# Performance work log

Hardware: AMD Instinct MI355X
Metric: run time of the kernel (lower is better)

The kernel has to match this reference:

```python
import jax, jax.numpy as jnp
import numpy as np

N0, N1, N2 = 100000, 25000, 6250
E0, E1, E2 = 600000, 150000, 40000
K = 6
NUM_CLASSES = 10


def setup_inputs() -> dict:
    key = jax.random.key(0)
    ks = jax.random.split(key, 20)
    inp = {
        "pos": jax.random.normal(ks[0], (N0, 3), dtype=jnp.float32),
        "edge_index0": jax.random.randint(ks[1], (2, E0), 0, N0, dtype=jnp.int32),
        "edge_index1": jax.random.randint(ks[2], (2, E1), 0, N1, dtype=jnp.int32),
        "edge_index2": jax.random.randint(ks[3], (2, E2), 0, N2, dtype=jnp.int32),
        "d0_rows": jax.random.randint(ks[4], (N0,), 0, N1, dtype=jnp.int32),
        "d0_cols": jax.random.randint(ks[5], (N0,), 0, N0, dtype=jnp.int32),
        "d0_vals": jax.random.uniform(ks[6], (N0,), dtype=jnp.float32),
        "d1_rows": jax.random.randint(ks[7], (N1,), 0, N2, dtype=jnp.int32),
        "d1_cols": jax.random.randint(ks[8], (N1,), 0, N1, dtype=jnp.int32),
        "d1_vals": jax.random.uniform(ks[9], (N1,), dtype=jnp.float32),
        "W0": jax.random.normal(ks[10], (K, 3, 32), dtype=jnp.float32) * 0.1,
        "b0": jax.random.normal(ks[11], (32,), dtype=jnp.float32) * 0.1,
        "W1": jax.random.normal(ks[12], (K, 32, 64), dtype=jnp.float32) * 0.1,
        "b1": jax.random.normal(ks[13], (64,), dtype=jnp.float32) * 0.1,
        "W2": jax.random.normal(ks[14], (K, 64, 128), dtype=jnp.float32) * 0.1,
        "b2": jax.random.normal(ks[15], (128,), dtype=jnp.float32) * 0.1,
        "lin_w": jax.random.normal(ks[16], (NUM_CLASSES, N2 * 128), dtype=jnp.float32) * 0.01,
        "lin_b": jax.random.normal(ks[17], (NUM_CLASSES,), dtype=jnp.float32) * 0.1,
    }
    return inp


def _cheb_edge_weights(row, col, n):
    # PyG get_laplacian(sym) followed by 2L/lambda_max - I with lambda_max=2:
    # diagonal becomes 0, off-diagonal weight = -deg^{-1/2}[row] * deg^{-1/2}[col]
    deg = jax.ops.segment_sum(jnp.ones(row.shape[0], jnp.float32), row, num_segments=n)
    dinv = jnp.where(deg > 0, 1.0 / jnp.sqrt(deg), 0.0)
    return -dinv[row] * dinv[col]


def _cheb_conv(x, edge_index, W, b, n):
    # Chebyshev recurrence: Tx0 = x, Tx1 = L_hat x, Tx_k = 2 L_hat Tx_{k-1} - Tx_{k-2}
    row, col = edge_index[0], edge_index[1]
    w = _cheb_edge_weights(row, col, n)

    def prop(z):  # [n, C] -> [n, C] scatter-gather over edges
        return jax.ops.segment_sum(w[:, None] * z[col], row, num_segments=n)

    Tx0 = x
    out = Tx0 @ W[0]
    Tx1 = prop(x)
    out = out + Tx1 @ W[1]
    for k in range(2, W.shape[0]):
        Tx2 = 2.0 * prop(Tx1) - Tx0
        out = out + Tx2 @ W[k]
        Tx0, Tx1 = Tx1, Tx2
    return out + b


def _pool(x, rows, cols, vals, n_out):
    # torch.sparse.mm(D, x) with D given in COO form
    return jax.ops.segment_sum(vals[:, None] * x[cols], rows, num_segments=n_out)


def reference(pos, edge_index0, edge_index1, edge_index2,
              d0_rows, d0_cols, d0_vals, d1_rows, d1_cols, d1_vals,
              W0, b0, W1, b1, W2, b2, lin_w, lin_b):
    x = jax.nn.relu(_cheb_conv(pos, edge_index0, W0, b0, N0))
    x = _pool(x, d0_rows, d0_cols, d0_vals, N1)
    x = jax.nn.relu(_cheb_conv(x, edge_index1, W1, b1, N1))
    x = _pool(x, d1_rows, d1_cols, d1_vals, N2)
    x = _cheb_conv(x, edge_index2, W2, b2, N2)  # no ReLU on last conv
    Z = lin_w @ x.reshape(-1) + lin_b
    return Z
```

## Files before the change

kernel.cpp:

```cpp
#include <hip/hip_runtime.h>


#define TPB 256
#define NB   318
#define BCAP 8192
#define EPB  4096
#define TXS  800000LL

static inline int gs(long long n) { return (int)((n + TPB - 1) / TPB); }

struct Desc5 {
    const int* rows[5];
    const int* cols[5];
    const float* vals[5];
    int eoff[6];
    int doff[5];
};


__global__ void k_binA_pad(Desc5 d, int* __restrict__ gbcnt, int2* __restrict__ binrec,
                           int Etot, int binBlocks,
                           const float* __restrict__ pos, float4* __restrict__ pdst,
                           int npos) {
    __shared__ int2 srec[EPB];
    __shared__ unsigned short sbuck[EPB];
    __shared__ int scnt[NB], sbase[NB], slcur[NB];
    int tid = threadIdx.x;
    if ((int)blockIdx.x >= binBlocks) {
        int i = (blockIdx.x - binBlocks) * 256 + tid;
        if (i < npos)
            pdst[i] = make_float4(pos[3 * i], pos[3 * i + 1], pos[3 * i + 2], 0.f);
        return;
    }
    int e0 = blockIdx.x * EPB;
    int ne = min(EPB, Etot - e0);
    for (int b = tid; b < NB; b += 256) scnt[b] = 0;
    __syncthreads();
    for (int i = tid; i < ne; i += 256) {
        int e = e0 + i;
        int s = 0;
        while (e >= d.eoff[s + 1]) ++s;
        int le = e - d.eoff[s];
        int grow = d.doff[s] + d.rows[s][le];
        int col = d.cols[s][le];
        int vb = (s >= 3) ? __float_as_int(d.vals[s][le]) : 0;
        int b = grow >> 9;
        srec[i] = make_int2(((grow & 511) << 17) | col, vb);
        sbuck[i] = (unsigned short)b;
        atomicAdd(&scnt[b], 1);
    }
    __syncthreads();
    for (int b = tid; b < NB; b += 256) {
        sbase[b] = scnt[b] > 0 ? atomicAdd(&gbcnt[b], scnt[b]) : 0;
        slcur[b] = 0;
    }
    __syncthreads();
    for (int i = tid; i < ne; i += 256) {
        int b = sbuck[i];
        int off = atomicAdd(&slcur[b], 1);
        binrec[(long long)b * BCAP + sbase[b] + off] = srec[i];
    }
}

__global__ void k_B1(const int* __restrict__ gbcnt, const int2* __restrict__ binrec,
                     int* __restrict__ rowptr, float* __restrict__ dinv,
                     int ntot, int ndinv, int Etot) {
    __shared__ int cnt[512], lexcl[512], wsum[4];
    int bucket = blockIdx.x, tid = threadIdx.x;
    int lane = tid & 63, wid = tid >> 6;
    {
        int v0 = (2 * tid < NB) ? gbcnt[2 * tid] : 0;
        int v1 = (2 * tid + 1 < NB) ? gbcnt[2 * tid + 1] : 0;
        int p = v0 + v1;
        int s = p;
#pragma unroll
        for (int off = 1; off < 64; off <<= 1) {
            int t = __shfl_up(s, off, 64);
            if (lane >= off) s += t;
        }
        if (lane == 63) wsum[wid] = s;
        __syncthreads();
        int add = 0;
        for (int w = 0; w < wid; ++w) add += wsum[w];
        int ep = add + s - p;
        lexcl[2 * tid] = ep; lexcl[2 * tid + 1] = ep + v0;
        __syncthreads();
    }
    int base = lexcl[bucket];
    __syncthreads();
    int ne = gbcnt[bucket];
    const int2* br = binrec + (long long)bucket * BCAP;
    cnt[2 * tid] = 0; cnt[2 * tid + 1] = 0;
    __syncthreads();
    for (int i = tid; i < ne; i += 256)
        atomicAdd(&cnt[br[i].x >> 17], 1);
    __syncthreads();
    int c0 = cnt[2 * tid], c1 = cnt[2 * tid + 1], p = c0 + c1;
    int s = p;
#pragma unroll
    for (int off = 1; off < 64; off <<= 1) {
        int t = __shfl_up(s, off, 64);
        if (lane >= off) s += t;
    }
    if (lane == 63) wsum[wid] = s;
    __syncthreads();
    int add = 0;
    for (int w = 0; w < wid; ++w) add += wsum[w];
    int ep = add + s - p;
    lexcl[2 * tid] = ep; lexcl[2 * tid + 1] = ep + c0;
    __syncthreads();
    int row0 = bucket << 9;
    int nrows = min(512, ntot - row0);
    for (int lr = tid; lr < nrows; lr += 256) {
        int grow = row0 + lr;
        rowptr[grow] = base + lexcl[lr];
        if (grow < ndinv) {
            int c = cnt[lr];
            dinv[grow] = c > 0 ? 1.0f / sqrtf((float)c) : 0.f;
        }
    }
    if (bucket == 0 && tid == 0) rowptr[ntot] = Etot;
}

__global__ void k_B2(const int* __restrict__ gbcnt, const int2* __restrict__ binrec,
                     const int* __restrict__ rowptr, const float* __restrict__ dinv,
                     int2* __restrict__ rec, int ntot) {
    __shared__ int lbase[512], lcur[512];
    int bucket = blockIdx.x, tid = threadIdx.x;
    int row0 = bucket << 9;
    for (int i = tid; i < 512; i += 256) {
        int grow = row0 + i;
        lbase[i] = (grow < ntot) ? rowptr[grow] : 0;
        lcur[i] = 0;
    }
    __syncthreads();
    int ne = gbcnt[bucket];
    const int2* br = binrec + (long long)bucket * BCAP;
    for (int i = tid; i < ne; i += 256) {
        int2 r = br[i];
        int lr = r.x >> 17, col = r.x & 0x1FFFF;
        int grow = row0 + lr;
        int pos = lbase[lr] + atomicAdd(&lcur[lr], 1);
        float wv;
        if (grow < 100000)      wv = dinv[col];
        else if (grow < 125000) wv = dinv[100000 + col];
        else if (grow < 131250) wv = dinv[125000 + col];
        else                    wv = __int_as_float(r.y);
        rec[pos] = make_int2(col, __float_as_int(wv));
    }
}


__global__ void k_sprop_c4p(const int* __restrict__ rowptr, const int2* __restrict__ rec,
                            const float* __restrict__ dinv, const float* __restrict__ src,
                            const float* __restrict__ prev, float* __restrict__ dst,
                            int n, int mode) {
    int idx = blockIdx.x * blockDim.x + threadIdx.x;
    if (idx >= 2 * n) return;
    int r = idx >> 1, half = idx & 1;
    int s0 = rowptr[r], s1 = rowptr[r + 1];
    float4 a0 = make_float4(0.f, 0.f, 0.f, 0.f), a1 = a0;
    int j = s0 + half;
    for (; j + 2 < s1; j += 4) {
        int2 r0 = rec[j], r1 = rec[j + 2];
        float w0 = __int_as_float(r0.y), w1 = __int_as_float(r1.y);
        float4 s0v = *(const float4*)(src + (long long)r0.x * 4);
        float4 s1v = *(const float4*)(src + (long long)r1.x * 4);
        a0.x += w0 * s0v.x; a0.y += w0 * s0v.y; a0.z += w0 * s0v.z; a0.w += w0 * s0v.w;
        a1.x += w1 * s1v.x; a1.y += w1 * s1v.y; a1.z += w1 * s1v.z; a1.w += w1 * s1v.w;
    }
    if (j < s1) {
        int2 rr = rec[j];
        float w = __int_as_float(rr.y);
        float4 s = *(const float4*)(src + (long long)rr.x * 4);
        a0.x += w * s.x; a0.y += w * s.y; a0.z += w * s.z; a0.w += w * s.w;
    }
    a0.x += a1.x; a0.y += a1.y; a0.z += a1.z; a0.w += a1.w;
    a0.x += __shfl_xor(a0.x, 1, 64);
    a0.y += __shfl_xor(a0.y, 1, 64);
    a0.z += __shfl_xor(a0.z, 1, 64);
    a0.w += __shfl_xor(a0.w, 1, 64);
    if (half == 0) {
        float m = -dinv[r];
        long long o = (long long)r * 4;
        float4 out;
        if (mode) {
            float4 p = *(const float4*)(prev + o);
            out.x = 2.f * m * a0.x - p.x; out.y = 2.f * m * a0.y - p.y;
            out.z = 2.f * m * a0.z - p.z; out.w = 2.f * m * a0.w - p.w;
        } else {
            out.x = m * a0.x; out.y = m * a0.y; out.z = m * a0.z; out.w = m * a0.w;
        }
        *(float4*)(dst + o) = out;
    }
}

__device__ __forceinline__
void sprop32p_body(const int* __restrict__ rowptr, const int2* __restrict__ rec,
                   const float* __restrict__ dinv, const float* __restrict__ src,
                   const float* __restrict__ prev, float* __restrict__ dst,
                   int n, int mode, int idx) {
    constexpr int C = 32;
    if (idx >= n * 8) return;
    int cid = idx >> 1, half = idx & 1;
    int r = cid >> 2, c4 = (cid & 3) * 8;
    int s0 = rowptr[r], s1 = rowptr[r + 1];
    float4 a0 = make_float4(0.f, 0.f, 0.f, 0.f), a1 = a0;
    for (int j = s0 + half; j < s1; j += 2) {
        int2 rr = rec[j];
        float w = __int_as_float(rr.y);
        const float* sp = src + (long long)rr.x * C + c4;
        float4 s0v = *(const float4*)(sp);
        float4 s1v = *(const float4*)(sp + 4);
        a0.x += w * s0v.x; a0.y += w * s0v.y; a0.z += w * s0v.z; a0.w += w * s0v.w;
        a1.x += w * s1v.x; a1.y += w * s1v.y; a1.z += w * s1v.z; a1.w += w * s1v.w;
    }
    a0.x += __shfl_xor(a0.x, 1, 64); a0.y += __shfl_xor(a0.y, 1, 64);
    a0.z += __shfl_xor(a0.z, 1, 64); a0.w += __shfl_xor(a0.w, 1, 64);
    a1.x += __shfl_xor(a1.x, 1, 64); a1.y += __shfl_xor(a1.y, 1, 64);
    a1.z += __shfl_xor(a1.z, 1, 64); a1.w += __shfl_xor(a1.w, 1, 64);
    if (half == 0) {
        float m = -dinv[r];
        long long o = (long long)r * C + c4;
        float4 o0, o1;
        if (mode) {
            float4 p0 = *(const float4*)(prev + o);
            float4 p1 = *(const float4*)(prev + o + 4);
            o0.x = 2.f * m * a0.x - p0.x; o0.y = 2.f * m * a0.y - p0.y;
            o0.z = 2.f * m * a0.z - p0.z; o0.w = 2.f * m * a0.w - p0.w;
            o1.x = 2.f * m * a1.x - p1.x; o1.y = 2.f * m * a1.y - p1.y;
            o1.z = 2.f * m * a1.z - p1.z; o1.w = 2.f * m * a1.w - p1.w;
        } else {
            o0.x = m * a0.x; o0.y = m * a0.y; o0.z = m * a0.z; o0.w = m * a0.w;
            o1.x = m * a1.x; o1.y = m * a1.y; o1.z = m * a1.z; o1.w = m * a1.w;
        }
        *(float4*)(dst + o) = o0;
        *(float4*)(dst + o + 4) = o1;
    }
}

__device__ __forceinline__
void sprop64p_body(const int* __restrict__ rowptr, const int2* __restrict__ rec,
                   const float* __restrict__ dinv, const float* __restrict__ src,
                   const float* __restrict__ prev, float* __restrict__ dst,
                   int n, int mode, int idx) {
    constexpr int C = 64, C4 = 16;
    if (idx >= n * C4 * 2) return;
    int cid = idx >> 1, half = idx & 1;
    int r = cid / C4, c4 = (cid - r * C4) * 4;
    int s0 = rowptr[r], s1 = rowptr[r + 1];
    float4 a0 = make_float4(0.f, 0.f, 0.f, 0.f), a1 = a0;
    int j = s0 + half;
    for (; j + 2 < s1; j += 4) {
        int2 r0 = rec[j], r1 = rec[j + 2];
        float w0 = __int_as_float(r0.y), w1 = __int_as_float(r1.y);
        float4 s0v = *(const float4*)(src + (long long)r0.x * C + c4);
        float4 s1v = *(const float4*)(src + (long long)r1.x * C + c4);
        a0.x += w0 * s0v.x; a0.y += w0 * s0v.y; a0.z += w0 * s0v.z; a0.w += w0 * s0v.w;
        a1.x += w1 * s1v.x; a1.y += w1 * s1v.y; a1.z += w1 * s1v.z; a1.w += w1 * s1v.w;
    }
    if (j < s1) {
        int2 rr = rec[j];
        float w = __int_as_float(rr.y);
        float4 s = *(const float4*)(src + (long long)rr.x * C + c4);
        a0.x += w * s.x; a0.y += w * s.y; a0.z += w * s.z; a0.w += w * s.w;
    }
    a0.x += a1.x; a0.y += a1.y; a0.z += a1.z; a0.w += a1.w;
    a0.x += __shfl_xor(a0.x, 1, 64); a0.y += __shfl_xor(a0.y, 1, 64);
    a0.z += __shfl_xor(a0.z, 1, 64); a0.w += __shfl_xor(a0.w, 1, 64);
    if (half == 0) {
        float m = -dinv[r];
        long long o = (long long)r * C + c4;
        float4 out;
        if (mode) {
            float4 p = *(const float4*)(prev + o);
            out.x = 2.f * m * a0.x - p.x; out.y = 2.f * m * a0.y - p.y;
            out.z = 2.f * m * a0.z - p.z; out.w = 2.f * m * a0.w - p.w;
        } else {
            out.x = m * a0.x; out.y = m * a0.y; out.z = m * a0.z; out.w = m * a0.w;
        }
        *(float4*)(dst + o) = out;
    }
}


template <int CIN, int COUT, int NT>
__device__ __forceinline__
void gemm1k_body(float* __restrict__ part, const float* __restrict__ txbase,
                 const float* __restrict__ W, int n, int pstride, int kg, int idx) {
    constexpr int CO4 = COUT / 4;
    int per = (n / NT) * CO4;
    if (idx >= per) return;
    int tile = idx / CO4, co = (idx - tile * CO4) * 4;
    int node0 = tile * NT;
    float4 acc[NT];
#pragma unroll
    for (int i = 0; i < NT; ++i) acc[i] = make_float4(0.f, 0.f, 0.f, 0.f);
    const float* xb = txbase + (long long)kg * TXS + (long long)node0 * CIN;
    const float* Wk = W + (long long)kg * CIN * COUT + co;
#pragma unroll 1
    for (int c4 = 0; c4 < CIN / 4; ++c4) {
        const float* Wr = Wk + c4 * 4 * COUT;
        float4 w0 = *(const float4*)(Wr);
        float4 w1 = *(const float4*)(Wr + COUT);
        float4 w2 = *(const float4*)(Wr + 2 * COUT);
        float4 w3 = *(const float4*)(Wr + 3 * COUT);
#pragma unroll
        for (int i = 0; i < NT; ++i) {
            float4 xv = *(const float4*)(xb + i * CIN + c4 * 4);
            acc[i].x += xv.x * w0.x + xv.y * w1.x + xv.z * w2.x + xv.w * w3.x;
            acc[i].y += xv.x * w0.y + xv.y * w1.y + xv.z * w2.y + xv.w * w3.y;
            acc[i].z += xv.x * w0.z + xv.y * w1.z + xv.z * w2.z + xv.w * w3.z;
            acc[i].w += xv.x * w0.w + xv.y * w1.w + xv.z * w2.w + xv.w * w3.w;
        }
    }
    float* op = part + (long long)kg * pstride + (long long)node0 * COUT + co;
#pragma unroll
    for (int i = 0; i < NT; ++i)
        *(float4*)(op + (long long)i * COUT) = acc[i];
}


__global__ __launch_bounds__(256, 4)
void k_pack1(const int* __restrict__ rowptr, const int2* __restrict__ rec,
             const float* __restrict__ dinv, const float* __restrict__ src,
             const float* __restrict__ prev, float* __restrict__ dst,
             int n, int mode, float* __restrict__ part,
             const float* __restrict__ txbase, const float* __restrict__ W,
             int pstride, int kg, int spropBlocks) {
    int bid = blockIdx.x;
    if (bid < spropBlocks)
        sprop32p_body(rowptr, rec, dinv, src, prev, dst, n, mode,
                      bid * 256 + threadIdx.x);
    else
        gemm1k_body<32, 64, 4>(part, txbase, W, n, pstride, kg,
                               (bid - spropBlocks) * 256 + threadIdx.x);
}

__global__ __launch_bounds__(256, 4)
void k_pack2(const int* __restrict__ rowptr, const int2* __restrict__ rec,
             const float* __restrict__ dinv, const float* __restrict__ src,
             const float* __restrict__ prev, float* __restrict__ dst,
             int n, int mode, float* __restrict__ part,
             const float* __restrict__ txbase, const float* __restrict__ W,
             int pstride, int kg, int spropBlocks) {
    int bid = blockIdx.x;
    if (bid < spropBlocks)
        sprop64p_body(rowptr, rec, dinv, src, prev, dst, n, mode,
                      bid * 256 + threadIdx.x);
    else
        gemm1k_body<64, 128, 2>(part, txbase, W, n, pstride, kg,
                                (bid - spropBlocks) * 256 + threadIdx.x);
}


__device__ __forceinline__
void convf1_body(const int* __restrict__ rowptr, const int2* __restrict__ rec,
                 const float* __restrict__ dinv, const float* __restrict__ txbase,
                 const float* __restrict__ W, float* __restrict__ part,
                 int n, int pstride, int bid, float (*ltx)[36]) {
    constexpr int C = 32;
    int tid = threadIdx.x;
    int row0 = bid * 32;
    const float* src = txbase + 4 * TXS;
    const float* prv = txbase + 3 * TXS;
    {
        int rl = tid >> 3, c4 = (tid & 7) * 4;
        int r = row0 + rl;
        if (r < n) {
            int s0 = rowptr[r], s1 = rowptr[r + 1];
            float4 a0 = make_float4(0.f, 0.f, 0.f, 0.f), a1 = a0;
            int j = s0;
            for (; j + 2 <= s1; j += 2) {
                int2 q0 = rec[j], q1 = rec[j + 1];
                float w0 = __int_as_float(q0.y), w1 = __int_as_float(q1.y);
                float4 s0v = *(const float4*)(src + (long long)q0.x * C + c4);
                float4 s1v = *(const float4*)(src + (long long)q1.x * C + c4);
                a0.x += w0 * s0v.x; a0.y += w0 * s0v.y; a0.z += w0 * s0v.z; a0.w += w0 * s0v.w;
                a1.x += w1 * s1v.x; a1.y += w1 * s1v.y; a1.z += w1 * s1v.z; a1.w += w1 * s1v.w;
            }
            if (j < s1) {
                int2 q = rec[j];
                float w = __int_as_float(q.y);
                float4 s = *(const float4*)(src + (long long)q.x * C + c4);
                a0.x += w * s.x; a0.y += w * s.y; a0.z += w * s.z; a0.w += w * s.w;
            }
            a0.x += a1.x; a0.y += a1.y; a0.z += a1.z; a0.w += a1.w;
            float m = -dinv[r];
            float4 p = *(const float4*)(prv + (long long)r * C + c4);
            ltx[rl][c4]     = 2.f * m * a0.x - p.x;
            ltx[rl][c4 + 1] = 2.f * m * a0.y - p.y;
            ltx[rl][c4 + 2] = 2.f * m * a0.z - p.z;
            ltx[rl][c4 + 3] = 2.f * m * a0.w - p.w;
        }
    }
    __syncthreads();
    const float* Wk = W + 5 * 32 * 64;
#pragma unroll
    for (int half = 0; half < 2; ++half) {
        int out_id = half * 256 + tid;
        int rl = out_id >> 4, co = (out_id & 15) * 4;
        int r = row0 + rl;
        if (r >= n) continue;
        float4 acc = make_float4(0.f, 0.f, 0.f, 0.f);
#pragma unroll 1
        for (int c4 = 0; c4 < 8; ++c4) {
            const float* Wr = Wk + c4 * 4 * 64 + co;
            float4 w0 = *(const float4*)(Wr);
            float4 w1 = *(const float4*)(Wr + 64);
            float4 w2 = *(const float4*)(Wr + 128);
            float4 w3 = *(const float4*)(Wr + 192);
            float4 xv = *(const float4*)(&ltx[rl][c4 * 4]);
            acc.x += xv.x * w0.x + xv.y * w1.x + xv.z * w2.x + xv.w * w3.x;
            acc.y += xv.x * w0.y + xv.y * w1.y + xv.z * w2.y + xv.w * w3.y;
            acc.z += xv.x * w0.z + xv.y * w1.z + xv.z * w2.z + xv.w * w3.z;
            acc.w += xv.x * w0.w + xv.y * w1.w + xv.z * w2.w + xv.w * w3.w;
        }
        *(float4*)(part + 5LL * pstride + (long long)r * 64 + co) = acc;
    }
}

__device__ __forceinline__
void convf2_body(const int* __restrict__ rowptr, const int2* __restrict__ rec,
                 const float* __restrict__ dinv, const float* __restrict__ txbase,
                 const float* __restrict__ W, float* __restrict__ part,
                 int n, int pstride, int bid, float (*ltx)[68]) {
    constexpr int C = 64;
    int tid = threadIdx.x;
    int row0 = bid * 16;
    const float* src = txbase + 4 * TXS;
    const float* prv = txbase + 3 * TXS;
    {
        int rl = tid >> 4, c4 = (tid & 15) * 4;
        int r = row0 + rl;
        if (r < n) {
            int s0 = rowptr[r], s1 = rowptr[r + 1];
            float4 a0 = make_float4(0.f, 0.f, 0.f, 0.f), a1 = a0;
            int j = s0;
            for (; j + 2 <= s1; j += 2) {
                int2 q0 = rec[j], q1 = rec[j + 1];
                float w0 = __int_as_float(q0.y), w1 = __int_as_float(q1.y);
                float4 s0v = *(const float4*)(src + (long long)q0.x * C + c4);
                float4 s1v = *(const float4*)(src + (long long)q1.x * C + c4);
                a0.x += w0 * s0v.x; a0.y += w0 * s0v.y; a0.z += w0 * s0v.z; a0.w += w0 * s0v.w;
                a1.x += w1 * s1v.x; a1.y += w1 * s1v.y; a1.z += w1 * s1v.z; a1.w += w1 * s1v.w;
            }
            if (j < s1) {
                int2 q = rec[j];
                float w = __int_as_float(q.y);
                float4 s = *(const float4*)(src + (long long)q.x * C + c4);
                a0.x += w * s.x; a0.y += w * s.y; a0.z += w * s.z; a0.w += w * s.w;
            }
            a0.x += a1.x; a0.y += a1.y; a0.z += a1.z; a0.w += a1.w;
            float m = -dinv[r];
            float4 p = *(const float4*)(prv + (long long)r * C + c4);
            ltx[rl][c4]     = 2.f * m * a0.x - p.x;
            ltx[rl][c4 + 1] = 2.f * m * a0.y - p.y;
            ltx[rl][c4 + 2] = 2.f * m * a0.z - p.z;
            ltx[rl][c4 + 3] = 2.f * m * a0.w - p.w;
        }
    }
    __syncthreads();
    const float* Wk = W + 5 * 64 * 128;
#pragma unroll
    for (int half = 0; half < 2; ++half) {
        int out_id = half * 256 + tid;
        int rl = out_id >> 5, co = (out_id & 31) * 4;
        int r = row0 + rl;
        if (r >= n) continue;
        float4 acc = make_float4(0.f, 0.f, 0.f, 0.f);
#pragma unroll 1
        for (int c4 = 0; c4 < 16; ++c4) {
            const float* Wr = Wk + c4 * 4 * 128 + co;
            float4 w0 = *(const float4*)(Wr);
            float4 w1 = *(const float4*)(Wr + 128);
            float4 w2 = *(const float4*)(Wr + 256);
            float4 w3 = *(const float4*)(Wr + 384);
            float4 xv = *(const float4*)(&ltx[rl][c4 * 4]);
            acc.x += xv.x * w0.x + xv.y * w1.x + xv.z * w2.x + xv.w * w3.x;
            acc.y += xv.x * w0.y + xv.y * w1.y + xv.z * w2.y + xv.w * w3.y;
            acc.z += xv.x * w0.z + xv.y * w1.z + xv.z * w2.z + xv.w * w3.z;
            acc.w += xv.x * w0.w + xv.y * w1.w + xv.z * w2.w + xv.w * w3.w;
        }
        *(float4*)(part + 5LL * pstride + (long long)r * 128 + co) = acc;
    }
}

__global__ __launch_bounds__(256, 4)
void k_packf1(const int* __restrict__ rowptr, const int2* __restrict__ rec,
              const float* __restrict__ dinv, const float* __restrict__ txbase,
              const float* __restrict__ W, float* __restrict__ part,
              int n, int pstride, int fB) {
    __shared__ float ltx[32][36];
    int bid = blockIdx.x;
    if (bid < fB)
        convf1_body(rowptr, rec, dinv, txbase, W, part, n, pstride, bid, ltx);
    else
        gemm1k_body<32, 64, 4>(part, txbase, W, n, pstride, 4,
                               (bid - fB) * 256 + threadIdx.x);
}

__global__ __launch_bounds__(256, 4)
void k_packf2(const int* __restrict__ rowptr, const int2* __restrict__ rec,
              const float* __restrict__ dinv, const float* __restrict__ txbase,
              const float* __restrict__ W, float* __restrict__ part,
              int n, int pstride, int fB) {
    __shared__ float ltx[16][68];
    int bid = blockIdx.x;
    if (bid < fB)
        convf2_body(rowptr, rec, dinv, txbase, W, part, n, pstride, bid, ltx);
    else
        gemm1k_body<64, 128, 2>(part, txbase, W, n, pstride, 4,
                                (bid - fB) * 256 + threadIdx.x);
}

__global__ __launch_bounds__(256, 4)
void k_conv0_final(const int* __restrict__ rowptr, const int2* __restrict__ rec,
                   const float* __restrict__ dinv, const float* __restrict__ txbase,
                   const float* __restrict__ W, const float* __restrict__ b,
                   float* __restrict__ out, int n) {
    int r = blockIdx.x * blockDim.x + threadIdx.x;
    if (r >= n) return;
    const float* src = txbase + 4 * TXS;
    int s0 = rowptr[r], s1 = rowptr[r + 1];
    float4 a0 = make_float4(0.f, 0.f, 0.f, 0.f);
    float4 a1 = a0;
    int j = s0;
    if ((j & 1) && j < s1) {
        int2 rr = rec[j];
        float w = __int_as_float(rr.y);
        float4 s = *(const float4*)(src + (long long)rr.x * 4);
        a0.x += w * s.x; a0.y += w * s.y; a0.z += w * s.z;
        ++j;
    }
    for (; j + 2 <= s1; j += 2) {
        int4 q = *(const int4*)(rec + j);
        float wa = __int_as_float(q.y), wb = __int_as_float(q.w);
        float4 sa = *(const float4*)(src + (long long)q.x * 4);
        float4 sb = *(const float4*)(src + (long long)q.z * 4);
        a0.x += wa * sa.x; a0.y += wa * sa.y; a0.z += wa * sa.z;
        a1.x += wb * sb.x; a1.y += wb * sb.y; a1.z += wb * sb.z;
    }
    if (j < s1) {
        int2 rr = rec[j];
        float w = __int_as_float(rr.y);
        float4 s = *(const float4*)(src + (long long)rr.x * 4);
        a0.x += w * s.x; a0.y += w * s.y; a0.z += w * s.z;
    }
    a0.x += a1.x; a0.y += a1.y; a0.z += a1.z;
    float m = -dinv[r];
    float4 xv[6];
#pragma unroll
    for (int k = 0; k < 5; ++k)
        xv[k] = *(const float4*)(txbase + (long long)k * TXS + (long long)r * 4);
    xv[5].x = 2.f * m * a0.x - xv[3].x;
    xv[5].y = 2.f * m * a0.y - xv[3].y;
    xv[5].z = 2.f * m * a0.z - xv[3].z;
    float* op = out + (long long)r * 32;
#pragma unroll 1
    for (int co4 = 0; co4 < 8; ++co4) {
        float4 acc = *(const float4*)(b + co4 * 4);
#pragma unroll
        for (int k = 0; k < 6; ++k) {
            const float* Wk = W + k * 96 + co4 * 4;
            float4 w0 = *(const float4*)(Wk);
            float4 w1 = *(const float4*)(Wk + 32);
            float4 w2 = *(const float4*)(Wk + 64);
            acc.x += xv[k].x * w0.x + xv[k].y * w1.x + xv[k].z * w2.x;
            acc.y += xv[k].x * w0.y + xv[k].y * w1.y + xv[k].z * w2.y;
            acc.z += xv[k].x * w0.z + xv[k].y * w1.z + xv[k].z * w2.z;
            acc.w += xv[k].x * w0.w + xv[k].y * w1.w + xv[k].z * w2.w;
        }
        *(float4*)(op + co4 * 4) = acc;
    }
}


template <int C>
__global__ void k_spool4_t(const int* __restrict__ rowptr, const int2* __restrict__ rec,
                           const float* __restrict__ x, float* __restrict__ out, int n) {
    constexpr int C4 = C / 4;
    int idx = blockIdx.x * blockDim.x + threadIdx.x;
    if (idx >= n * C4) return;
    int r = idx / C4, c4 = (idx - r * C4) * 4;
    int s0 = rowptr[r], s1 = rowptr[r + 1];
    float4 acca = make_float4(0.f, 0.f, 0.f, 0.f);
    float4 accb = make_float4(0.f, 0.f, 0.f, 0.f);
    int j = s0;
    if ((j & 1) && j < s1) {
        int2 rr = rec[j];
        float v = __int_as_float(rr.y);
        float4 s = *(const float4*)(x + (long long)rr.x * C + c4);
        acca.x += v * fmaxf(s.x, 0.f); acca.y += v * fmaxf(s.y, 0.f);
        acca.z += v * fmaxf(s.z, 0.f); acca.w += v * fmaxf(s.w, 0.f);
        ++j;
    }
    for (; j + 2 <= s1; j += 2) {
        int4 q = *(const int4*)(rec + j);
        float va = __int_as_float(q.y), vb = __int_as_float(q.w);
        float4 sa = *(const float4*)(x + (long long)q.x * C + c4);
        float4 sb = *(const float4*)(x + (long long)q.z * C + c4);
        acca.x += va * fmaxf(sa.x, 0.f); acca.y += va * fmaxf(sa.y, 0.f);
        acca.z += va * fmaxf(sa.z, 0.f); acca.w += va * fmaxf(sa.w, 0.f);
        accb.x += vb * fmaxf(sb.x, 0.f); accb.y += vb * fmaxf(sb.y, 0.f);
        accb.z += vb * fmaxf(sb.z, 0.f); accb.w += vb * fmaxf(sb.w, 0.f);
    }
    if (j < s1) {
        int2 rr = rec[j];
        float v = __int_as_float(rr.y);
        float4 s = *(const float4*)(x + (long long)rr.x * C + c4);
        acca.x += v * fmaxf(s.x, 0.f); acca.y += v * fmaxf(s.y, 0.f);
        acca.z += v * fmaxf(s.z, 0.f); acca.w += v * fmaxf(s.w, 0.f);
    }
    acca.x += accb.x; acca.y += accb.y; acca.z += accb.z; acca.w += accb.w;
    *(float4*)(out + (long long)r * C + c4) = acca;
}


template <int C, int KSPLIT>
__global__ void k_pool_f(const int* __restrict__ rowptr, const int2* __restrict__ rec,
                         const float* __restrict__ part, const float* __restrict__ bias,
                         float* __restrict__ out, int n, int partStride) {
    constexpr int C4 = C / 4;
    int idx = blockIdx.x * blockDim.x + threadIdx.x;
    if (idx >= n * C4) return;
    int r = idx / C4, c4 = (idx - r * C4) * 4;
    int s0 = rowptr[r], s1 = rowptr[r + 1];
    float4 bb = *(const float4*)(bias + c4);
    float4 acc = make_float4(0.f, 0.f, 0.f, 0.f);
    for (int j = s0; j < s1; ++j) {
        int2 rr = rec[j];
        float v = __int_as_float(rr.y);
        float4 x = bb;
#pragma unroll
        for (int s = 0; s < KSPLIT; ++s) {
            float4 p = *(const float4*)(part + (long long)s * partStride + (long long)rr.x * C + c4);
            x.x += p.x; x.y += p.y; x.z += p.z; x.w += p.w;
        }
        acc.x += v * fmaxf(x.x, 0.f); acc.y += v * fmaxf(x.y, 0.f);
        acc.z += v * fmaxf(x.z, 0.f); acc.w += v * fmaxf(x.w, 0.f);
    }
    *(float4*)(out + (long long)r * C + c4) = acc;
}


__global__ void k_linear_partial_f(const float* __restrict__ lw,
                                   const float4* __restrict__ part,
                                   const float* __restrict__ b2,
                                   float* __restrict__ partials,
                                   int len4, int len, int nblk) {
    float acc[10];
#pragma unroll
    for (int j = 0; j < 10; ++j) acc[j] = 0.f;
    const float4* b2v = (const float4*)b2;
    for (int i = blockIdx.x * blockDim.x + threadIdx.x; i < len4;
         i += gridDim.x * blockDim.x) {
        float4 xv = b2v[i & 31];
#pragma unroll
        for (int s = 0; s < 6; ++s) {
            float4 p = part[s * 200000 + i];
            xv.x += p.x; xv.y += p.y; xv.z += p.z; xv.w += p.w;
        }
#pragma unroll
        for (int j = 0; j < 10; ++j) {
            float4 wv = *(const float4*)(lw + (long long)j * len + i * 4);
            acc[j] += xv.x * wv.x + xv.y * wv.y + xv.z * wv.z + xv.w * wv.w;
        }
    }
    __shared__ float lds[4][10];
    int wid = threadIdx.x >> 6, lane = threadIdx.x & 63;
#pragma unroll
    for (int j = 0; j < 10; ++j) {
        float v = acc[j];
        for (int off = 32; off > 0; off >>= 1) v += __shfl_down(v, off, 64);
        if (lane == 0) lds[wid][j] = v;
    }
    __syncthreads();
    if (threadIdx.x < 10) {
        float s = lds[0][threadIdx.x] + lds[1][threadIdx.x] +
                  lds[2][threadIdx.x] + lds[3][threadIdx.x];
        partials[threadIdx.x * nblk + blockIdx.x] = s;
    }
}

__global__ void k_linear_final(const float* __restrict__ partials,
                               const float* __restrict__ lb,
                               float* __restrict__ out, int nblk) {
    int j = threadIdx.x >> 6, lane = threadIdx.x & 63;
    float v = 0.f;
    for (int b = lane; b < nblk; b += 64) v += partials[j * nblk + b];
    for (int off = 32; off > 0; off >>= 1) v += __shfl_down(v, off, 64);
    if (lane == 0) out[j] = lb[j] + v;
}

extern "C" void kernel_launch(void* const* d_in, const int* in_sizes, int n_in,
                              void* d_out, int out_size, void* d_ws, size_t ws_size,
                              hipStream_t stream) {
    const int cN0 = 100000, cN1 = 25000, cN2 = 6250;
    const int cE0 = 600000, cE1 = 150000, cE2 = 40000;
    const int NBLK = 512;

    const float* pos = (const float*)d_in[0];
    const int*   ei0 = (const int*)d_in[1];
    const int*   ei1 = (const int*)d_in[2];
    const int*   ei2 = (const int*)d_in[3];
    const int*   d0r = (const int*)d_in[4];
    const int*   d0c = (const int*)d_in[5];
    const float* d0v = (const float*)d_in[6];
    const int*   d1r = (const int*)d_in[7];
    const int*   d1c = (const int*)d_in[8];
    const float* d1v = (const float*)d_in[9];
    const float* W0  = (const float*)d_in[10];
    const float* b0  = (const float*)d_in[11];
    const float* W1  = (const float*)d_in[12];
    const float* b1  = (const float*)d_in[13];
    const float* W2  = (const float*)d_in[14];
    const float* b2  = (const float*)d_in[15];
    const float* lw  = (const float*)d_in[16];
    const float* lb  = (const float*)d_in[17];
    float* outZ = (float*)d_out;

    const int ntot = cN0 + cN1 + cN2 + cN1 + cN2;
    const int Etot = cE0 + cE1 + cE2 + cN0 + cN1;
    const int Eg   = cE0 + cE1 + cE2;
    const int ndinv = cN0 + cN1 + cN2;
    const int doff0 = 0, doff1 = cN0, doff2 = cN0 + cN1,
              doffp0 = doff2 + cN2, doffp1 = doffp0 + cN1;

    int*   iws    = (int*)d_ws;
    int*   gbcnt  = iws;
    int*   rowptr = gbcnt + 320;
    float* dinv   = (float*)(rowptr + 162504);
    int2*  binrec = (int2*)(dinv + 131256);
    int2*  rec    = binrec + (long long)NB * BCAP;
    float* txbuf  = (float*)(rec + 915000);
    float* part   = txbuf + 6 * TXS;
    float* bufOut = part + 9600000;
    float* lpart  = bufOut + 3200000;

    Desc5 d;
    d.rows[0] = ei0;        d.cols[0] = ei0 + cE0; d.vals[0] = nullptr;
    d.rows[1] = ei1;        d.cols[1] = ei1 + cE1; d.vals[1] = nullptr;
    d.rows[2] = ei2;        d.cols[2] = ei2 + cE2; d.vals[2] = nullptr;
    d.rows[3] = d0r;        d.cols[3] = d0c;       d.vals[3] = d0v;
    d.rows[4] = d1r;        d.cols[4] = d1c;       d.vals[4] = d1v;
    d.eoff[0] = 0;
    d.eoff[1] = cE0;
    d.eoff[2] = cE0 + cE1;
    d.eoff[3] = Eg;
    d.eoff[4] = Eg + cN0;
    d.eoff[5] = Etot;
    d.doff[0] = doff0; d.doff[1] = doff1; d.doff[2] = doff2;
    d.doff[3] = doffp0; d.doff[4] = doffp1;

    hipMemsetAsync(gbcnt, 0, (size_t)NB * 4, stream);
    int binBlocks = (Etot + EPB - 1) / EPB;
    int padBlocks = gs(cN0);
    k_binA_pad<<<binBlocks + padBlocks, TPB, 0, stream>>>(
        d, gbcnt, binrec, Etot, binBlocks, pos, (float4*)txbuf, cN0);
    k_B1<<<NB, TPB, 0, stream>>>(gbcnt, binrec, rowptr, dinv, ntot, ndinv, Etot);
    k_B2<<<NB, TPB, 0, stream>>>(gbcnt, binrec, rowptr, dinv, rec, ntot);

    for (int k = 1; k <= 4; ++k) {
        const float* src = txbuf + (long long)(k - 1) * TXS;
        const float* prev = (k >= 2) ? txbuf + (long long)(k - 2) * TXS : nullptr;
        float* dst = txbuf + (long long)k * TXS;
        k_sprop_c4p<<<gs((long long)cN0 * 2), TPB, 0, stream>>>(
            rowptr + doff0, rec, dinv + doff0, src, prev, dst, cN0, k >= 2 ? 1 : 0);
    }
    k_conv0_final<<<gs(cN0), TPB, 0, stream>>>(
        rowptr + doff0, rec, dinv + doff0, txbuf, W0, b0, bufOut, cN0);
    k_spool4_t<32><<<gs((long long)cN1 * 8), TPB, 0, stream>>>(
        rowptr + doffp0, rec, bufOut, txbuf, cN1);

    {
        const int pstride = cN1 * 64;
        int sB = gs((long long)cN1 * 8);
        int gB = gs((long long)(cN1 / 4) * 16);
        for (int k = 1; k <= 4; ++k) {
            const float* src = txbuf + (long long)(k - 1) * TXS;
            const float* prev = (k >= 2) ? txbuf + (long long)(k - 2) * TXS : nullptr;
            float* dst = txbuf + (long long)k * TXS;
            k_pack1<<<sB + gB, TPB, 0, stream>>>(
                rowptr + doff1, rec, dinv + doff1, src, prev, dst, cN1,
                k >= 2 ? 1 : 0, part, txbuf, W1, pstride, k - 1, sB);
        }
        int fB = (cN1 + 31) / 32;
        k_packf1<<<fB + gB, TPB, 0, stream>>>(
            rowptr + doff1, rec, dinv + doff1, txbuf, W1, part, cN1, pstride, fB);
        k_pool_f<64, 6><<<gs((long long)cN2 * 16), TPB, 0, stream>>>(
            rowptr + doffp1, rec, part, b1, txbuf, cN2, pstride);
    }

    {
        const int pstride = cN2 * 128;
        int sB = gs((long long)cN2 * 32);
        int gB = gs((long long)(cN2 / 2) * 32);
        for (int k = 1; k <= 4; ++k) {
            const float* src = txbuf + (long long)(k - 1) * TXS;
            const float* prev = (k >= 2) ? txbuf + (long long)(k - 2) * TXS : nullptr;
            float* dst = txbuf + (long long)k * TXS;
            k_pack2<<<sB + gB, TPB, 0, stream>>>(
                rowptr + doff2, rec, dinv + doff2, src, prev, dst, cN2,
                k >= 2 ? 1 : 0, part, txbuf, W2, pstride, k - 1, sB);
        }
        int fB = (cN2 + 15) / 16;
        k_packf2<<<fB + gB, TPB, 0, stream>>>(
            rowptr + doff2, rec, dinv + doff2, txbuf, W2, part, cN2, pstride, fB);
        k_linear_partial_f<<<NBLK, TPB, 0, stream>>>(
            lw, (const float4*)part, b2, lpart, cN2 * 128 / 4, cN2 * 128, NBLK);
        k_linear_final<<<1, 640, 0, stream>>>(lpart, lb, outZ, NBLK);
    }
}
```

Measured before the change: 253.0 us.

## Overlap tail of CSR record build with first level-0 propagation; fuse linear reduction

The record-scatter kernel is split so that the buckets past B2SPLIT (which hold later graph levels and pooling records) run in the same launch as the first Chebyshev propagation for level 0. This overlaps the two kernels' work and removes one launch. The final linear layer now does its cross-block reduction in a last-block-done pattern using an atomic counter, replacing the separate single-block final kernel. The overlap depends on level-0 rows living entirely in buckets below B2SPLIT, and the counter needs the widened memset.

```diff
diff --git a/kernel.cpp b/kernel.cpp
--- a/kernel.cpp
+++ b/kernel.cpp
@@ -6,6 +6,7 @@
 #define BCAP 8192
 #define EPB  4096
 #define TXS  800000LL
+#define B2SPLIT 196
 
 static inline int gs(long long n) { return (int)((n + TPB - 1) / TPB); }
 
@@ -122,11 +123,12 @@
     if (bucket == 0 && tid == 0) rowptr[ntot] = Etot;
 }
 
-__global__ void k_B2(const int* __restrict__ gbcnt, const int2* __restrict__ binrec,
-                     const int* __restrict__ rowptr, const float* __restrict__ dinv,
-                     int2* __restrict__ rec, int ntot) {
+__device__ __forceinline__
+void b2_body(const int* __restrict__ gbcnt, const int2* __restrict__ binrec,
+             const int* __restrict__ rowptr, const float* __restrict__ dinv,
+             int2* __restrict__ rec, int ntot, int bucket) {
     __shared__ int lbase[512], lcur[512];
-    int bucket = blockIdx.x, tid = threadIdx.x;
+    int tid = threadIdx.x;
     int row0 = bucket << 9;
     for (int i = tid; i < 512; i += 256) {
         int grow = row0 + i;
@@ -150,12 +152,18 @@
     }
 }
 
-
-__global__ void k_sprop_c4p(const int* __restrict__ rowptr, const int2* __restrict__ rec,
-                            const float* __restrict__ dinv, const float* __restrict__ src,
-                            const float* __restrict__ prev, float* __restrict__ dst,
-                            int n, int mode) {
-    int idx = blockIdx.x * blockDim.x + threadIdx.x;
+__global__ void k_B2a(const int* __restrict__ gbcnt, const int2* __restrict__ binrec,
+                      const int* __restrict__ rowptr, const float* __restrict__ dinv,
+                      int2* __restrict__ rec, int ntot) {
+    b2_body(gbcnt, binrec, rowptr, dinv, rec, ntot, blockIdx.x);
+}
+
+
+__device__ __forceinline__
+void sprop_c4p_body(const int* __restrict__ rowptr, const int2* __restrict__ rec,
+                    const float* __restrict__ dinv, const float* __restrict__ src,
+                    const float* __restrict__ prev, float* __restrict__ dst,
+                    int n, int mode, int idx) {
     if (idx >= 2 * n) return;
     int r = idx >> 1, half = idx & 1;
     int s0 = rowptr[r], s1 = rowptr[r + 1];
@@ -193,6 +201,28 @@
         }
         *(float4*)(dst + o) = out;
     }
+}
+
+__global__ void k_sprop_c4p(const int* __restrict__ rowptr, const int2* __restrict__ rec,
+                            const float* __restrict__ dinv, const float* __restrict__ src,
+                            const float* __restrict__ prev, float* __restrict__ dst,
+                            int n, int mode) {
+    sprop_c4p_body(rowptr, rec, dinv, src, prev, dst, n, mode,
+                   blockIdx.x * blockDim.x + threadIdx.x);
+}
+
+__global__ void k_h1b2(const int* __restrict__ rowptr, const int2* __restrict__ rec,
+                       const float* __restrict__ dinv, const float* __restrict__ src,
+                       float* __restrict__ dst, int n, int hB,
+                       const int* __restrict__ gbcnt, const int2* __restrict__ binrec,
+                       const int* __restrict__ rowptr_all, int ntot) {
+    int bid = blockIdx.x;
+    if (bid < hB)
+        sprop_c4p_body(rowptr, rec, dinv, src, nullptr, dst, n, 0,
+                       bid * 256 + threadIdx.x);
+    else
+        b2_body(gbcnt, binrec, rowptr_all, dinv, (int2*)rec, ntot,
+                B2SPLIT + (bid - hB));
 }
 
 __device__ __forceinline__
@@ -644,11 +674,14 @@
 }
 
 
-__global__ void k_linear_partial_f(const float* __restrict__ lw,
-                                   const float4* __restrict__ part,
-                                   const float* __restrict__ b2,
-                                   float* __restrict__ partials,
-                                   int len4, int len, int nblk) {
+__global__ void k_linear_fused(const float* __restrict__ lw,
+                               const float4* __restrict__ part,
+                               const float* __restrict__ b2,
+                               const float* __restrict__ lb,
+                               float* __restrict__ partials,
+                               int* __restrict__ cnt,
+                               float* __restrict__ out,
+                               int len4, int len, int nblk) {
     float acc[10];
 #pragma unroll
     for (int j = 0; j < 10; ++j) acc[j] = 0.f;
@@ -668,6 +701,7 @@
         }
     }
     __shared__ float lds[4][10];
+    __shared__ int isLast;
     int wid = threadIdx.x >> 6, lane = threadIdx.x & 63;
 #pragma unroll
     for (int j = 0; j < 10; ++j) {
@@ -681,16 +715,24 @@
                   lds[2][threadIdx.x] + lds[3][threadIdx.x];
         partials[threadIdx.x * nblk + blockIdx.x] = s;
     }
-}
-
-__global__ void k_linear_final(const float* __restrict__ partials,
-                               const float* __restrict__ lb,
-                               float* __restrict__ out, int nblk) {
-    int j = threadIdx.x >> 6, lane = threadIdx.x & 63;
-    float v = 0.f;
-    for (int b = lane; b < nblk; b += 64) v += partials[j * nblk + b];
-    for (int off = 32; off > 0; off >>= 1) v += __shfl_down(v, off, 64);
-    if (lane == 0) out[j] = lb[j] + v;
+    __threadfence();
+    __syncthreads();
+    if (threadIdx.x == 0)
+        isLast = (atomicAdd(cnt, 1) == nblk - 1) ? 1 : 0;
+    __syncthreads();
+    if (!isLast) return;
+    __threadfence();
+    for (int j = 0; j < 10; ++j) {
+        float v = 0.f;
+        for (int i = threadIdx.x; i < nblk; i += 256)
+            v += partials[j * nblk + i];
+        for (int off = 32; off > 0; off >>= 1) v += __shfl_down(v, off, 64);
+        if (lane == 0) lds[wid][0] = v;
+        __syncthreads();
+        if (threadIdx.x == 0)
+            out[j] = lb[j] + lds[0][0] + lds[1][0] + lds[2][0] + lds[3][0];
+        __syncthreads();
+    }
 }
 
 extern "C" void kernel_launch(void* const* d_in, const int* in_sizes, int n_in,
@@ -729,6 +771,7 @@
 
     int*   iws    = (int*)d_ws;
     int*   gbcnt  = iws;
+    int*   lpcnt  = gbcnt + 318;
     int*   rowptr = gbcnt + 320;
     float* dinv   = (float*)(rowptr + 162504);
     int2*  binrec = (int2*)(dinv + 131256);
@@ -753,20 +796,26 @@
     d.doff[0] = doff0; d.doff[1] = doff1; d.doff[2] = doff2;
     d.doff[3] = doffp0; d.doff[4] = doffp1;
 
-    hipMemsetAsync(gbcnt, 0, (size_t)NB * 4, stream);
+    hipMemsetAsync(gbcnt, 0, (size_t)320 * 4, stream);
     int binBlocks = (Etot + EPB - 1) / EPB;
     int padBlocks = gs(cN0);
     k_binA_pad<<<binBlocks + padBlocks, TPB, 0, stream>>>(
         d, gbcnt, binrec, Etot, binBlocks, pos, (float4*)txbuf, cN0);
     k_B1<<<NB, TPB, 0, stream>>>(gbcnt, binrec, rowptr, dinv, ntot, ndinv, Etot);
-    k_B2<<<NB, TPB, 0, stream>>>(gbcnt, binrec, rowptr, dinv, rec, ntot);
-
-    for (int k = 1; k <= 4; ++k) {
+    k_B2a<<<B2SPLIT, TPB, 0, stream>>>(gbcnt, binrec, rowptr, dinv, rec, ntot);
+
+    {
+        int hB = gs((long long)cN0 * 2);
+        k_h1b2<<<hB + (NB - B2SPLIT), TPB, 0, stream>>>(
+            rowptr + doff0, rec, dinv + doff0, txbuf, txbuf + TXS, cN0, hB,
+            gbcnt, binrec, rowptr, ntot);
+    }
+    for (int k = 2; k <= 4; ++k) {
         const float* src = txbuf + (long long)(k - 1) * TXS;
-        const float* prev = (k >= 2) ? txbuf + (long long)(k - 2) * TXS : nullptr;
+        const float* prev = txbuf + (long long)(k - 2) * TXS;
         float* dst = txbuf + (long long)k * TXS;
         k_sprop_c4p<<<gs((long long)cN0 * 2), TPB, 0, stream>>>(
-            rowptr + doff0, rec, dinv + doff0, src, prev, dst, cN0, k >= 2 ? 1 : 0);
+            rowptr + doff0, rec, dinv + doff0, src, prev, dst, cN0, 1);
     }
     k_conv0_final<<<gs(cN0), TPB, 0, stream>>>(
         rowptr + doff0, rec, dinv + doff0, txbuf, W0, b0, bufOut, cN0);
@@ -807,8 +856,8 @@
         int fB = (cN2 + 15) / 16;
         k_packf2<<<fB + gB, TPB, 0, stream>>>(
             rowptr + doff2, rec, dinv + doff2, txbuf, W2, part, cN2, pstride, fB);
-        k_linear_partial_f<<<NBLK, TPB, 0, stream>>>(
-            lw, (const float4*)part, b2, lpart, cN2 * 128 / 4, cN2 * 128, NBLK);
-        k_linear_final<<<1, 640, 0, stream>>>(lpart, lb, outZ, NBLK);
-    }
-}
+        k_linear_fused<<<NBLK, TPB, 0, stream>>>(
+            lw, (const float4*)part, b2, lb, lpart, lpcnt, outZ,
+            cN2 * 128 / 4, cN2 * 128, NBLK);
+    }
+}
```

Measured after the change: 297.3 us. 17.5% more time.
